# Performance work log

Measured on AMD Instinct MI355X. Metric: run time of the kernel, lower is better.

The kernel has to match this reference:

```python
import jax, jax.numpy as jnp
import numpy as np

DEPTH, DIM, HEADS, DH, MLP = 2, 512, 8, 64, 2048
INNER = HEADS * DH
B, L = 2, 2048
SCALE = DH ** -0.5
LN_EPS = 1e-5


def setup_inputs() -> dict:
    key = jax.random.key(0)
    ks = jax.random.split(key, 8)
    s = 0.02
    return {
        "x": jax.random.normal(ks[0], (B, L, DIM), dtype=jnp.float32),
        "mask": jax.random.randint(ks[1], (B, L, L), 0, 2, dtype=jnp.int32),
        "ln1_g": jnp.ones((DEPTH, DIM), jnp.float32),
        "ln1_b": jnp.zeros((DEPTH, DIM), jnp.float32),
        "w_qkv": jax.random.normal(ks[2], (DEPTH, DIM, 3 * INNER), jnp.float32) * s,
        "w_out": jax.random.normal(ks[3], (DEPTH, INNER, DIM), jnp.float32) * s,
        "b_out": jnp.zeros((DEPTH, DIM), jnp.float32),
        "ln2_g": jnp.ones((DEPTH, DIM), jnp.float32),
        "ln2_b": jnp.zeros((DEPTH, DIM), jnp.float32),
        "w1": jax.random.normal(ks[4], (DEPTH, DIM, MLP), jnp.float32) * s,
        "b1": jnp.zeros((DEPTH, MLP), jnp.float32),
        "w2": jax.random.normal(ks[5], (DEPTH, MLP, DIM), jnp.float32) * s,
        "b2": jnp.zeros((DEPTH, DIM), jnp.float32),
    }


def _layer_norm(x, g, b):
    m = jnp.mean(x, axis=-1, keepdims=True)
    v = jnp.mean(jnp.square(x - m), axis=-1, keepdims=True)
    return (x - m) * jax.lax.rsqrt(v + LN_EPS) * g + b


def _attention(h, mask_f, w_qkv, w_out, b_out):
    b, l, _ = h.shape
    qkv = h @ w_qkv  # [b,l,3*inner]
    qkv = qkv.reshape(b, l, 3, HEADS, DH)
    q = jnp.transpose(qkv[:, :, 0], (0, 2, 1, 3))  # [b,h,l,dh]
    k = jnp.transpose(qkv[:, :, 1], (0, 2, 1, 3))
    v = jnp.transpose(qkv[:, :, 2], (0, 2, 1, 3))
    scores = jnp.einsum('bhqd,bhkd->bhqk', q, k) * SCALE
    attn = jax.nn.softmax(scores, axis=-1)
    # multiplicative mask + renormalization (non-standard)
    attn = attn * mask_f
    attn = attn / (jnp.sum(attn, axis=-1, keepdims=True) + 1e-10)
    z = jnp.einsum('bhqk,bhkd->bhqd', attn, v)
    z = jnp.transpose(z, (0, 2, 1, 3)).reshape(b, l, INNER)
    return z @ w_out + b_out


def reference(x, mask, ln1_g, ln1_b, w_qkv, w_out, b_out, ln2_g, ln2_b, w1, b1, w2, b2):
    mask_f = mask[:, None, :, :].astype(x.dtype)  # [b,1,l,l]
    h = x
    for d in range(DEPTH):
        a = _attention(_layer_norm(h, ln1_g[d], ln1_b[d]), mask_f,
                       w_qkv[d], w_out[d], b_out[d])
        h = h + a
        f = _layer_norm(h, ln2_g[d], ln2_b[d])
        f = jax.nn.gelu(f @ w1[d] + b1[d], approximate=False) @ w2[d] + b2[d]
        h = h + f
    return h
```

## Files before the change

kernel.cpp:

```cpp
#include <hip/hip_runtime.h>
#include <math.h>

#define DEPTH 2
#define DIM   512
#define HEADS 8
#define DH    64
#define INNER 512
#define MLP_D 2048
#define BSZ   2
#define SEQ   2048
#define MROWS (BSZ*SEQ)
#define SCALE 0.125f
#define LN_EPS 1e-5f

typedef unsigned short u16;
typedef unsigned int   u32;
typedef __attribute__((ext_vector_type(8))) unsigned short u16x8;
typedef __attribute__((ext_vector_type(4))) unsigned short u16x4;
typedef __attribute__((ext_vector_type(8))) short          s16x8;
typedef __attribute__((ext_vector_type(4))) float          f32x4;

__device__ __forceinline__ u16 f2bf(float f) {
    u32 u = __float_as_uint(f);
    u += 0x7fffu + ((u >> 16) & 1u);
    return (u16)(u >> 16);
}

__device__ __forceinline__ float wred_sum(float v) {
    #pragma unroll
    for (int o = 32; o; o >>= 1) v += __shfl_xor(v, o);
    return v;
}

__global__ __launch_bounds__(256) void ln_kernel(
    const float* __restrict__ x,
    const float* __restrict__ g,
    const float* __restrict__ b,
    u16* __restrict__ y)
{
    const int wave = threadIdx.x >> 6;
    const int lane = threadIdx.x & 63;
    const int row  = blockIdx.x * 4 + wave;
    const float* xr = x + (size_t)row * DIM;

    float4 v0 = *reinterpret_cast<const float4*>(&xr[lane * 8]);
    float4 v1 = *reinterpret_cast<const float4*>(&xr[lane * 8 + 4]);

    float s = v0.x + v0.y + v0.z + v0.w + v1.x + v1.y + v1.z + v1.w;
    s = wred_sum(s);
    const float mean = s * (1.0f / DIM);

    float d[8] = {v0.x - mean, v0.y - mean, v0.z - mean, v0.w - mean,
                  v1.x - mean, v1.y - mean, v1.z - mean, v1.w - mean};
    float ss = 0.f;
    #pragma unroll
    for (int i = 0; i < 8; ++i) ss += d[i] * d[i];
    ss = wred_sum(ss);
    const float inv = rsqrtf(ss * (1.0f / DIM) + LN_EPS);

    float4 g0 = *reinterpret_cast<const float4*>(&g[lane * 8]);
    float4 g1 = *reinterpret_cast<const float4*>(&g[lane * 8 + 4]);
    float4 b0 = *reinterpret_cast<const float4*>(&b[lane * 8]);
    float4 b1 = *reinterpret_cast<const float4*>(&b[lane * 8 + 4]);
    const float gg[8] = {g0.x, g0.y, g0.z, g0.w, g1.x, g1.y, g1.z, g1.w};
    const float bb[8] = {b0.x, b0.y, b0.z, b0.w, b1.x, b1.y, b1.z, b1.w};

    u16x8 o;
    #pragma unroll
    for (int i = 0; i < 8; ++i) o[i] = f2bf(d[i] * inv * gg[i] + bb[i]);
    *reinterpret_cast<u16x8*>(&y[(size_t)row * DIM + lane * 8]) = o;
}

__global__ __launch_bounds__(256) void transpose_bf16_kernel(
    const float* __restrict__ in, u16* __restrict__ out, int K, int N)
{
    __shared__ u16 t[64][65];
    const int k0 = blockIdx.y * 64, n0 = blockIdx.x * 64;
    const int tid = threadIdx.x;
    #pragma unroll
    for (int i = 0; i < 4; ++i) {
        int idx = tid + i * 256;
        int r = idx >> 4, c4 = idx & 15;
        float4 v = *reinterpret_cast<const float4*>(&in[(size_t)(k0 + r) * N + n0 + c4 * 4]);
        t[c4 * 4 + 0][r] = f2bf(v.x);
        t[c4 * 4 + 1][r] = f2bf(v.y);
        t[c4 * 4 + 2][r] = f2bf(v.z);
        t[c4 * 4 + 3][r] = f2bf(v.w);
    }
    __syncthreads();
    #pragma unroll
    for (int i = 0; i < 2; ++i) {
        int idx = tid + i * 256;
        int r = idx >> 3, c8 = idx & 7;
        u16x8 w;
        #pragma unroll
        for (int j = 0; j < 8; ++j) w[j] = t[r][c8 * 8 + j];
        *reinterpret_cast<u16x8*>(&out[(size_t)(n0 + r) * K + k0 + c8 * 8]) = w;
    }
}

__global__ __launch_bounds__(256) void mask_pack_kernel(
    const int* __restrict__ mask, u32* __restrict__ mbT)
{
    const int wv = threadIdx.x >> 6, lane = threadIdx.x & 63;
    const int row = blockIdx.x * 4 + wv;
    const int b = row >> 11, l = row & (SEQ - 1);
    const int* mr = mask + (size_t)row * SEQ;
    u32* out = mbT + (size_t)b * 64 * SEQ;
    for (int it = 0; it < 32; ++it) {
        unsigned long long bal = __ballot(mr[it * 64 + lane] != 0);
        if (lane == 0) {
            out[(size_t)(2 * it) * SEQ + l]     = (u32)bal;
            out[(size_t)(2 * it + 1) * SEQ + l] = (u32)(bal >> 32);
        }
    }
}

template<int BM, int BN, int MT, int NT, int EPI>
__global__ __launch_bounds__(256) void gemm_bf16(
    const u16* __restrict__ A, const u16* __restrict__ BT,
    const float* __restrict__ bias, const float* __restrict__ Cin,
    void* __restrict__ CoutV, u16* __restrict__ qo, u16* __restrict__ ko,
    u16* __restrict__ vo, int M, int N, int K)
{
    constexpr int BK = 32;
    constexpr int LDW = 40;
    constexpr int WC = BN / (NT * 16);
    constexpr int AR = (BM * BK) / (256 * 8);
    constexpr int BR = (BN * BK) / (256 * 8);

    __shared__ __align__(16) u16 As[BM * LDW];
    __shared__ __align__(16) u16 Bs[BN * LDW];

    const int tid  = threadIdx.x;
    const int lane = tid & 63;
    const int wid  = tid >> 6;
    const int wr   = wid / WC, wc = wid % WC;
    const int lr   = lane & 15, lk = lane >> 4;
    const int bm   = blockIdx.y * BM, bn = blockIdx.x * BN;

    f32x4 acc[MT][NT];
    #pragma unroll
    for (int i = 0; i < MT; ++i)
        #pragma unroll
        for (int j = 0; j < NT; ++j) {
            acc[i][j][0] = 0.f; acc[i][j][1] = 0.f;
            acc[i][j][2] = 0.f; acc[i][j][3] = 0.f;
        }

    u16x8 ar[AR], br[BR];
    #pragma unroll
    for (int i = 0; i < AR; ++i) {
        int idx = tid + i * 256, row = idx >> 2, k16 = idx & 3;
        ar[i] = *reinterpret_cast<const u16x8*>(&A[(size_t)(bm + row) * K + k16 * 8]);
    }
    #pragma unroll
    for (int i = 0; i < BR; ++i) {
        int idx = tid + i * 256, row = idx >> 2, k16 = idx & 3;
        br[i] = *reinterpret_cast<const u16x8*>(&BT[(size_t)(bn + row) * K + k16 * 8]);
    }

    const int NTILES = K / BK;
    for (int t = 0; t < NTILES; ++t) {
        __syncthreads();
        #pragma unroll
        for (int i = 0; i < AR; ++i) {
            int idx = tid + i * 256, row = idx >> 2, k16 = idx & 3;
            *reinterpret_cast<u16x8*>(&As[row * LDW + k16 * 8]) = ar[i];
        }
        #pragma unroll
        for (int i = 0; i < BR; ++i) {
            int idx = tid + i * 256, row = idx >> 2, k16 = idx & 3;
            *reinterpret_cast<u16x8*>(&Bs[row * LDW + k16 * 8]) = br[i];
        }
        __syncthreads();

        if (t + 1 < NTILES) {
            const int k0 = (t + 1) * BK;
            #pragma unroll
            for (int i = 0; i < AR; ++i) {
                int idx = tid + i * 256, row = idx >> 2, k16 = idx & 3;
                ar[i] = *reinterpret_cast<const u16x8*>(&A[(size_t)(bm + row) * K + k0 + k16 * 8]);
            }
            #pragma unroll
            for (int i = 0; i < BR; ++i) {
                int idx = tid + i * 256, row = idx >> 2, k16 = idx & 3;
                br[i] = *reinterpret_cast<const u16x8*>(&BT[(size_t)(bn + row) * K + k0 + k16 * 8]);
            }
        }

        s16x8 af[MT], bf[NT];
        #pragma unroll
        for (int mt = 0; mt < MT; ++mt)
            af[mt] = *reinterpret_cast<const s16x8*>(&As[(wr * MT * 16 + mt * 16 + lr) * LDW + lk * 8]);
        #pragma unroll
        for (int nt = 0; nt < NT; ++nt)
            bf[nt] = *reinterpret_cast<const s16x8*>(&Bs[(wc * NT * 16 + nt * 16 + lr) * LDW + lk * 8]);
        #pragma unroll
        for (int mt = 0; mt < MT; ++mt)
            #pragma unroll
            for (int nt = 0; nt < NT; ++nt)
                acc[mt][nt] = __builtin_amdgcn_mfma_f32_16x16x32_bf16(
                    af[mt], bf[nt], acc[mt][nt], 0, 0, 0);
    }

    if (EPI == 3) {
        #pragma unroll
        for (int mt = 0; mt < MT; ++mt) {
            const int rbase = bm + wr * MT * 16 + mt * 16 + lk * 4;
            #pragma unroll
            for (int nt = 0; nt < NT; ++nt) {
                const int c = bn + wc * NT * 16 + nt * 16 + lr;
                const int sec = c >> 9, hh = (c >> 6) & 7, dd = c & 63;
                if (sec == 0) {
                    #pragma unroll
                    for (int i = 0; i < 4; ++i)
                        qo[((size_t)hh * MROWS + rbase + i) * 64 + dd] =
                            f2bf(acc[mt][nt][i] * SCALE);
                } else if (sec == 1) {
                    #pragma unroll
                    for (int i = 0; i < 4; ++i)
                        ko[((size_t)hh * MROWS + rbase + i) * 64 + dd] =
                            f2bf(acc[mt][nt][i]);
                } else {
                    u16x4 o;
                    #pragma unroll
                    for (int i = 0; i < 4; ++i) o[i] = f2bf(acc[mt][nt][i]);
                    *reinterpret_cast<u16x4*>(
                        &vo[((size_t)hh * 64 + dd) * MROWS + rbase]) = o;
                }
            }
        }
        return;
    }
    #pragma unroll
    for (int mt = 0; mt < MT; ++mt) {
        #pragma unroll
        for (int i = 0; i < 4; ++i) {
            const size_t r = bm + wr * MT * 16 + mt * 16 + lk * 4 + i;
            #pragma unroll
            for (int nt = 0; nt < NT; ++nt) {
                const size_t c = bn + wc * NT * 16 + nt * 16 + lr;
                float v = acc[mt][nt][i];
                if (EPI == 1) {
                    v += bias[c];
                    v = 0.5f * v * (1.0f + erff(v * 0.70710678118654752f));
                    ((u16*)CoutV)[r * N + c] = f2bf(v);
                } else {
                    v += bias[c] + Cin[r * N + c];
                    ((float*)CoutV)[r * N + c] = v;
                }
            }
        }
    }
}

__global__ __launch_bounds__(256) void attn_mfma_kernel(
    const u16* __restrict__ Qb,
    const u16* __restrict__ Kb,
    const u16* __restrict__ Vtb,
    const u32* __restrict__ mbT,
    u16* __restrict__ z)
{
    const int bh = blockIdx.y;
    const int b = bh >> 3, h = bh & 7;
    const int q0 = blockIdx.x * 64;
    const int tid = threadIdx.x;
    const int w = tid >> 6, lane = tid & 63;
    const int lr = lane & 15, lk = lane >> 4;

    __shared__ __align__(16) u16 Ks[128 * 72];
    __shared__ __align__(16) u16 Vts[64 * 136];

    const int qrow = q0 + w * 16 + lr;
    const size_t qg = (size_t)b * SEQ + qrow;

    s16x8 qf0, qf1;
    {
        const u16* Qrow = Qb + ((size_t)h * MROWS + qg) * 64;
        qf0 = *reinterpret_cast<const s16x8*>(Qrow + lk * 8);
        qf1 = *reinterpret_cast<const s16x8*>(Qrow + 32 + lk * 8);
    }

    float Mx = -1e30f, Sa = 0.f, Sm = 0.f;
    f32x4 zacc[4];
    #pragma unroll
    for (int dt = 0; dt < 4; ++dt) {
        zacc[dt][0] = 0.f; zacc[dt][1] = 0.f; zacc[dt][2] = 0.f; zacc[dt][3] = 0.f;
    }

    const u16* Kbase = Kb + ((size_t)h * MROWS + (size_t)b * SEQ) * 64;
    const u16* Vbase = Vtb + (size_t)h * 64 * MROWS + (size_t)b * SEQ;
    const u32* mbase = mbT + (size_t)b * 64 * SEQ;

    for (int kv0 = 0; kv0 < SEQ; kv0 += 128) {
        u16x8 kr[4], vr[4];
        #pragma unroll
        for (int i = 0; i < 4; ++i) {
            int idx = tid + i * 256;
            int row = idx >> 3, c8 = idx & 7;
            kr[i] = *reinterpret_cast<const u16x8*>(
                Kbase + (size_t)(kv0 + row) * 64 + c8 * 8);
        }
        #pragma unroll
        for (int i = 0; i < 4; ++i) {
            int idx = tid + i * 256;
            int row = idx >> 4, c = idx & 15;
            vr[i] = *reinterpret_cast<const u16x8*>(
                Vbase + (size_t)row * MROWS + kv0 + c * 8);
        }
        u32 mw[4];
        #pragma unroll
        for (int j = 0; j < 4; ++j)
            mw[j] = mbase[(size_t)(kv0 / 32 + j) * SEQ + qrow];

        __syncthreads();
        #pragma unroll
        for (int i = 0; i < 4; ++i) {
            int idx = tid + i * 256;
            int row = idx >> 3, c8 = idx & 7;
            *reinterpret_cast<u16x8*>(&Ks[row * 72 + c8 * 8]) = kr[i];
        }
        #pragma unroll
        for (int i = 0; i < 4; ++i) {
            int idx = tid + i * 256;
            int row = idx >> 4, c = idx & 15;
            *reinterpret_cast<u16x8*>(&Vts[row * 136 + c * 8]) = vr[i];
        }
        __syncthreads();

        f32x4 st[8];
        #pragma unroll
        for (int mt = 0; mt < 8; ++mt) {
            st[mt][0] = 0.f; st[mt][1] = 0.f; st[mt][2] = 0.f; st[mt][3] = 0.f;
        }
        #pragma unroll
        for (int mt = 0; mt < 8; ++mt) {
            const s16x8 a0 = *reinterpret_cast<const s16x8*>(
                &Ks[(mt * 16 + lr) * 72 + lk * 8]);
            const s16x8 a1 = *reinterpret_cast<const s16x8*>(
                &Ks[(mt * 16 + lr) * 72 + 32 + lk * 8]);
            st[mt] = __builtin_amdgcn_mfma_f32_16x16x32_bf16(a0, qf0, st[mt], 0, 0, 0);
            st[mt] = __builtin_amdgcn_mfma_f32_16x16x32_bf16(a1, qf1, st[mt], 0, 0, 0);
        }

        float ml = -1e30f;
        #pragma unroll
        for (int mt = 0; mt < 8; ++mt)
            #pragma unroll
            for (int i = 0; i < 4; ++i) ml = fmaxf(ml, st[mt][i]);
        ml = fmaxf(ml, __shfl_xor(ml, 16));
        ml = fmaxf(ml, __shfl_xor(ml, 32));
        const float Mn = fmaxf(Mx, ml);
        const float rsc = __expf(Mx - Mn);
        Mx = Mn;

        float ta = 0.f, tm = 0.f;
        #pragma unroll
        for (int mt = 0; mt < 8; ++mt) {
            const u32 wsh = mw[mt >> 1] >> ((mt & 1) * 16 + lk * 4);
            #pragma unroll
            for (int i = 0; i < 4; ++i) {
                float e = __expf(st[mt][i] - Mn);
                ta += e;
                float em = ((wsh >> i) & 1u) ? e : 0.f;
                tm += em;
                st[mt][i] = em;
            }
        }
        ta += __shfl_xor(ta, 16); ta += __shfl_xor(ta, 32);
        tm += __shfl_xor(tm, 16); tm += __shfl_xor(tm, 32);
        Sa = Sa * rsc + ta;
        Sm = Sm * rsc + tm;
        #pragma unroll
        for (int dt = 0; dt < 4; ++dt)
            #pragma unroll
            for (int i = 0; i < 4; ++i) zacc[dt][i] *= rsc;

        #pragma unroll
        for (int s = 0; s < 4; ++s) {
            s16x8 pf;
            #pragma unroll
            for (int i = 0; i < 4; ++i) {
                pf[i]     = (short)f2bf(st[2 * s][i]);
                pf[i + 4] = (short)f2bf(st[2 * s + 1][i]);
            }
            #pragma unroll
            for (int dt = 0; dt < 4; ++dt) {
                const u16* vrow = &Vts[(dt * 16 + lr) * 136 + s * 32 + lk * 4];
                u16x4 v0 = *reinterpret_cast<const u16x4*>(vrow);
                u16x4 v1 = *reinterpret_cast<const u16x4*>(vrow + 16);
                s16x8 av;
                #pragma unroll
                for (int i = 0; i < 4; ++i) {
                    av[i]     = (short)v0[i];
                    av[i + 4] = (short)v1[i];
                }
                zacc[dt] = __builtin_amdgcn_mfma_f32_16x16x32_bf16(av, pf, zacc[dt], 0, 0, 0);
            }
        }
    }

    const float inv = 1.0f / (Sm + 1e-10f * Sa);
    #pragma unroll
    for (int dt = 0; dt < 4; ++dt) {
        u16x4 o;
        #pragma unroll
        for (int i = 0; i < 4; ++i) o[i] = f2bf(zacc[dt][i] * inv);
        *reinterpret_cast<u16x4*>(
            &z[qg * INNER + h * 64 + dt * 16 + lk * 4]) = o;
    }
}

extern "C" void kernel_launch(void* const* d_in, const int* in_sizes, int n_in,
                              void* d_out, int out_size, void* d_ws, size_t ws_size,
                              hipStream_t stream) {
    const float* x      = (const float*)d_in[0];
    const int*   mask   = (const int*)  d_in[1];
    const float* ln1_g  = (const float*)d_in[2];
    const float* ln1_b  = (const float*)d_in[3];
    const float* w_qkv  = (const float*)d_in[4];
    const float* w_out  = (const float*)d_in[5];
    const float* b_out  = (const float*)d_in[6];
    const float* ln2_g  = (const float*)d_in[7];
    const float* ln2_b  = (const float*)d_in[8];
    const float* w1     = (const float*)d_in[9];
    const float* b1     = (const float*)d_in[10];
    const float* w2     = (const float*)d_in[11];
    const float* b2     = (const float*)d_in[12];

    float* h = (float*)d_out;

    u16* hn  = (u16*)d_ws;
    u16* zb  = hn + (size_t)MROWS * DIM;
    u32* mbT = (u32*)(zb + (size_t)MROWS * DIM);
    u16* wT  = (u16*)(mbT + (size_t)BSZ * 64 * SEQ);
    const size_t WT_LAYER = (size_t)DIM * 3 * INNER + (size_t)INNER * DIM
                          + (size_t)DIM * MLP_D + (size_t)MLP_D * DIM;
    u16* big = wT + DEPTH * WT_LAYER;
    u16* Qb  = big;
    u16* Kb  = Qb + (size_t)HEADS * MROWS * 64;
    u16* Vtb = Kb + (size_t)HEADS * MROWS * 64;
    u16* f1  = big;

    hipMemcpyAsync(h, x, (size_t)MROWS * DIM * sizeof(float),
                   hipMemcpyDeviceToDevice, stream);

    mask_pack_kernel<<<MROWS / 4, 256, 0, stream>>>(mask, mbT);
    for (int d = 0; d < DEPTH; ++d) {
        u16* wqkvT = wT + d * WT_LAYER;
        u16* woutT = wqkvT + (size_t)3 * INNER * DIM;
        u16* w1T   = woutT + (size_t)DIM * INNER;
        u16* w2T   = w1T   + (size_t)MLP_D * DIM;
        transpose_bf16_kernel<<<dim3(3 * INNER / 64, DIM / 64), 256, 0, stream>>>(
            w_qkv + (size_t)d * DIM * 3 * INNER, wqkvT, DIM, 3 * INNER);
        transpose_bf16_kernel<<<dim3(INNER / 64, DIM / 64), 256, 0, stream>>>(
            w_out + (size_t)d * INNER * DIM, woutT, INNER, DIM);
        transpose_bf16_kernel<<<dim3(MLP_D / 64, DIM / 64), 256, 0, stream>>>(
            w1 + (size_t)d * DIM * MLP_D, w1T, DIM, MLP_D);
        transpose_bf16_kernel<<<dim3(DIM / 64, MLP_D / 64), 256, 0, stream>>>(
            w2 + (size_t)d * MLP_D * DIM, w2T, MLP_D, DIM);
    }

    for (int d = 0; d < DEPTH; ++d) {
        u16* wqkvT = wT + d * WT_LAYER;
        u16* woutT = wqkvT + (size_t)3 * INNER * DIM;
        u16* w1T   = woutT + (size_t)DIM * INNER;
        u16* w2T   = w1T   + (size_t)MLP_D * DIM;

        ln_kernel<<<MROWS / 4, 256, 0, stream>>>(h, ln1_g + d * DIM, ln1_b + d * DIM, hn);

        gemm_bf16<128, 128, 4, 4, 3><<<dim3(3 * INNER / 128, MROWS / 128), 256, 0, stream>>>(
            hn, wqkvT, nullptr, nullptr, nullptr, Qb, Kb, Vtb, MROWS, 3 * INNER, DIM);

        attn_mfma_kernel<<<dim3(SEQ / 64, BSZ * HEADS), 256, 0, stream>>>(
            Qb, Kb, Vtb, mbT, zb);

        gemm_bf16<128, 64, 4, 2, 2><<<dim3(DIM / 64, MROWS / 128), 256, 0, stream>>>(
            zb, woutT, b_out + d * DIM, h, h, nullptr, nullptr, nullptr, MROWS, DIM, INNER);

        ln_kernel<<<MROWS / 4, 256, 0, stream>>>(h, ln2_g + d * DIM, ln2_b + d * DIM, hn);

        gemm_bf16<128, 128, 4, 4, 1><<<dim3(MLP_D / 128, MROWS / 128), 256, 0, stream>>>(
            hn, w1T, b1 + d * MLP_D, nullptr, f1, nullptr, nullptr, nullptr, MROWS, MLP_D, DIM);

        gemm_bf16<128, 64, 4, 2, 2><<<dim3(DIM / 64, MROWS / 128), 256, 0, stream>>>(
            f1, w2T, b2 + d * DIM, h, h, nullptr, nullptr, nullptr, MROWS, DIM, MLP_D);
    }
}
```

Baseline: 430.1 us.

## Double-buffer GEMM and attention tiles via direct global-to-LDS loads

GEMM and attention kernels now load tiles straight from global memory into LDS with global_load_lds into two buffers, so the next tile's loads overlap compute on the current one. K and V tiles use an XOR swizzle instead of padding, and V is stored in a permuted order so each MFMA operand comes from one 16-byte LDS read. Softmax moves to exp2 with log2e folded into the Q scale, rescales lazily only when the max grows by more than a threshold, uses packed bf16 conversion, and drops the unmasked sum from the denominator. That last change alters the epsilon term of the renormalisation, and the lazy rescale leaves exponentials unnormalised by up to 2^8.

```diff
diff --git a/kernel.cpp b/kernel.cpp
--- a/kernel.cpp
+++ b/kernel.cpp
@@ -11,6 +11,7 @@
 #define SEQ   2048
 #define MROWS (BSZ*SEQ)
 #define SCALE 0.125f
+#define QSC   0.18033688f
 #define LN_EPS 1e-5f
 
 typedef unsigned short u16;
@@ -25,6 +26,16 @@
     u += 0x7fffu + ((u >> 16) & 1u);
     return (u16)(u >> 16);
 }
+__device__ __forceinline__ u32 cvtpk(float lo, float hi) {
+    u32 r;
+    asm("v_cvt_pk_bf16_f32 %0, %1, %2" : "=v"(r) : "v"(lo), "v"(hi));
+    return r;
+}
+__device__ __forceinline__ void gld16(const void* g, void* l) {
+    __builtin_amdgcn_global_load_lds(
+        (const __attribute__((address_space(1))) void*)g,
+        (__attribute__((address_space(3))) void*)l, 16, 0, 0);
+}
 
 __device__ __forceinline__ float wred_sum(float v) {
     #pragma unroll
@@ -33,10 +44,8 @@
 }
 
 __global__ __launch_bounds__(256) void ln_kernel(
-    const float* __restrict__ x,
-    const float* __restrict__ g,
-    const float* __restrict__ b,
-    u16* __restrict__ y)
+    const float* __restrict__ x, const float* __restrict__ g,
+    const float* __restrict__ b, u16* __restrict__ y)
 {
     const int wave = threadIdx.x >> 6;
     const int lane = threadIdx.x & 63;
@@ -116,6 +125,22 @@
     }
 }
 
+#define GSTAGE(buf, kt) do {                                                   \
+    const int k0_ = (kt) * BK;                                                 \
+    _Pragma("unroll")                                                          \
+    for (int i_ = 0; i_ < ACH; ++i_) {                                         \
+        int idx_ = i_ * 256 + tid; int r_ = idx_ >> 2, kc_ = idx_ & 3;         \
+        gld16(&A[(size_t)(bm + r_) * K + k0_ + kc_ * 8],                       \
+              &As[buf][(size_t)(i_ * 256 + (wid << 6)) * 8]);                  \
+    }                                                                          \
+    _Pragma("unroll")                                                          \
+    for (int i_ = 0; i_ < BCH; ++i_) {                                         \
+        int idx_ = i_ * 256 + tid; int r_ = idx_ >> 2, kc_ = idx_ & 3;         \
+        gld16(&BT[(size_t)(bn + r_) * K + k0_ + kc_ * 8],                      \
+              &Bs[buf][(size_t)(i_ * 256 + (wid << 6)) * 8]);                  \
+    }                                                                          \
+} while (0)
+
 template<int BM, int BN, int MT, int NT, int EPI>
 __global__ __launch_bounds__(256) void gemm_bf16(
     const u16* __restrict__ A, const u16* __restrict__ BT,
@@ -124,20 +149,18 @@
     u16* __restrict__ vo, int M, int N, int K)
 {
     constexpr int BK = 32;
-    constexpr int LDW = 40;
     constexpr int WC = BN / (NT * 16);
-    constexpr int AR = (BM * BK) / (256 * 8);
-    constexpr int BR = (BN * BK) / (256 * 8);
-
-    __shared__ __align__(16) u16 As[BM * LDW];
-    __shared__ __align__(16) u16 Bs[BN * LDW];
+    constexpr int ACH = (BM * BK) / (256 * 8);
+    constexpr int BCH = (BN * BK) / (256 * 8);
+
+    __shared__ __align__(16) u16 As[2][BM * BK];
+    __shared__ __align__(16) u16 Bs[2][BN * BK];
 
     const int tid  = threadIdx.x;
-    const int lane = tid & 63;
-    const int wid  = tid >> 6;
-    const int wr   = wid / WC, wc = wid % WC;
-    const int lr   = lane & 15, lk = lane >> 4;
-    const int bm   = blockIdx.y * BM, bn = blockIdx.x * BN;
+    const int lane = tid & 63, wid = tid >> 6;
+    const int wr = wid / WC, wc = wid % WC;
+    const int lr = lane & 15, lk = lane >> 4;
+    const int bm = blockIdx.y * BM, bn = blockIdx.x * BN;
 
     f32x4 acc[MT][NT];
     #pragma unroll
@@ -148,60 +171,34 @@
             acc[i][j][2] = 0.f; acc[i][j][3] = 0.f;
         }
 
-    u16x8 ar[AR], br[BR];
-    #pragma unroll
-    for (int i = 0; i < AR; ++i) {
-        int idx = tid + i * 256, row = idx >> 2, k16 = idx & 3;
-        ar[i] = *reinterpret_cast<const u16x8*>(&A[(size_t)(bm + row) * K + k16 * 8]);
-    }
-    #pragma unroll
-    for (int i = 0; i < BR; ++i) {
-        int idx = tid + i * 256, row = idx >> 2, k16 = idx & 3;
-        br[i] = *reinterpret_cast<const u16x8*>(&BT[(size_t)(bn + row) * K + k16 * 8]);
-    }
+    GSTAGE(0, 0);
+    asm volatile("s_waitcnt vmcnt(0)" ::: "memory");
+    __syncthreads();
 
     const int NTILES = K / BK;
+    int cur = 0;
     for (int t = 0; t < NTILES; ++t) {
-        __syncthreads();
-        #pragma unroll
-        for (int i = 0; i < AR; ++i) {
-            int idx = tid + i * 256, row = idx >> 2, k16 = idx & 3;
-            *reinterpret_cast<u16x8*>(&As[row * LDW + k16 * 8]) = ar[i];
-        }
-        #pragma unroll
-        for (int i = 0; i < BR; ++i) {
-            int idx = tid + i * 256, row = idx >> 2, k16 = idx & 3;
-            *reinterpret_cast<u16x8*>(&Bs[row * LDW + k16 * 8]) = br[i];
-        }
-        __syncthreads();
-
-        if (t + 1 < NTILES) {
-            const int k0 = (t + 1) * BK;
-            #pragma unroll
-            for (int i = 0; i < AR; ++i) {
-                int idx = tid + i * 256, row = idx >> 2, k16 = idx & 3;
-                ar[i] = *reinterpret_cast<const u16x8*>(&A[(size_t)(bm + row) * K + k0 + k16 * 8]);
-            }
-            #pragma unroll
-            for (int i = 0; i < BR; ++i) {
-                int idx = tid + i * 256, row = idx >> 2, k16 = idx & 3;
-                br[i] = *reinterpret_cast<const u16x8*>(&BT[(size_t)(bn + row) * K + k0 + k16 * 8]);
-            }
-        }
+        if (t + 1 < NTILES) GSTAGE(cur ^ 1, t + 1);
 
         s16x8 af[MT], bf[NT];
         #pragma unroll
         for (int mt = 0; mt < MT; ++mt)
-            af[mt] = *reinterpret_cast<const s16x8*>(&As[(wr * MT * 16 + mt * 16 + lr) * LDW + lk * 8]);
+            af[mt] = *reinterpret_cast<const s16x8*>(
+                &As[cur][(wr * MT * 16 + mt * 16 + lr) * BK + lk * 8]);
         #pragma unroll
         for (int nt = 0; nt < NT; ++nt)
-            bf[nt] = *reinterpret_cast<const s16x8*>(&Bs[(wc * NT * 16 + nt * 16 + lr) * LDW + lk * 8]);
+            bf[nt] = *reinterpret_cast<const s16x8*>(
+                &Bs[cur][(wc * NT * 16 + nt * 16 + lr) * BK + lk * 8]);
         #pragma unroll
         for (int mt = 0; mt < MT; ++mt)
             #pragma unroll
             for (int nt = 0; nt < NT; ++nt)
                 acc[mt][nt] = __builtin_amdgcn_mfma_f32_16x16x32_bf16(
                     af[mt], bf[nt], acc[mt][nt], 0, 0, 0);
+
+        asm volatile("s_waitcnt vmcnt(0)" ::: "memory");
+        __syncthreads();
+        cur ^= 1;
     }
 
     if (EPI == 3) {
@@ -216,18 +213,19 @@
                     #pragma unroll
                     for (int i = 0; i < 4; ++i)
                         qo[((size_t)hh * MROWS + rbase + i) * 64 + dd] =
-                            f2bf(acc[mt][nt][i] * SCALE);
+                            f2bf(acc[mt][nt][i] * QSC);
                 } else if (sec == 1) {
                     #pragma unroll
                     for (int i = 0; i < 4; ++i)
                         ko[((size_t)hh * MROWS + rbase + i) * 64 + dd] =
                             f2bf(acc[mt][nt][i]);
                 } else {
+                    const int pos = (rbase & ~31) + lk * 8 + (mt & 1) * 4;
                     u16x4 o;
                     #pragma unroll
                     for (int i = 0; i < 4; ++i) o[i] = f2bf(acc[mt][nt][i]);
                     *reinterpret_cast<u16x4*>(
-                        &vo[((size_t)hh * 64 + dd) * MROWS + rbase]) = o;
+                        &vo[((size_t)hh * 64 + dd) * MROWS + pos]) = o;
                 }
             }
         }
@@ -254,6 +252,22 @@
         }
     }
 }
+#undef GSTAGE
+
+#define ASTAGE(buf, kv) do {                                                   \
+    _Pragma("unroll")                                                          \
+    for (int i_ = 0; i_ < 4; ++i_) {                                           \
+        int idx_ = i_ * 256 + tid; int r_ = idx_ >> 3, c_ = idx_ & 7;          \
+        gld16(Kbase + (size_t)((kv) + r_) * 64 + ((c_ ^ (r_ & 7)) * 8),        \
+              &Ks[buf][(size_t)(i_ * 256 + (wid << 6)) * 8]);                  \
+    }                                                                          \
+    _Pragma("unroll")                                                          \
+    for (int i_ = 0; i_ < 4; ++i_) {                                           \
+        int idx_ = i_ * 256 + tid; int r_ = idx_ >> 4, c_ = idx_ & 15;         \
+        gld16(Vbase + (size_t)r_ * MROWS + (kv) + ((c_ ^ (r_ & 7)) * 8),       \
+              &Vts[buf][(size_t)(i_ * 256 + (wid << 6)) * 8]);                 \
+    }                                                                          \
+} while (0)
 
 __global__ __launch_bounds__(256) void attn_mfma_kernel(
     const u16* __restrict__ Qb,
@@ -266,13 +280,14 @@
     const int b = bh >> 3, h = bh & 7;
     const int q0 = blockIdx.x * 64;
     const int tid = threadIdx.x;
-    const int w = tid >> 6, lane = tid & 63;
+    const int wid = tid >> 6, lane = tid & 63;
     const int lr = lane & 15, lk = lane >> 4;
-
-    __shared__ __align__(16) u16 Ks[128 * 72];
-    __shared__ __align__(16) u16 Vts[64 * 136];
-
-    const int qrow = q0 + w * 16 + lr;
+    const int lr7 = lr & 7;
+
+    __shared__ __align__(16) u16 Ks[2][128 * 64];
+    __shared__ __align__(16) u16 Vts[2][64 * 128];
+
+    const int qrow = q0 + wid * 16 + lr;
     const size_t qg = (size_t)b * SEQ + qrow;
 
     s16x8 qf0, qf1;
@@ -282,7 +297,7 @@
         qf1 = *reinterpret_cast<const s16x8*>(Qrow + 32 + lk * 8);
     }
 
-    float Mx = -1e30f, Sa = 0.f, Sm = 0.f;
+    float Mx = -1e30f, Sm = 0.f;
     f32x4 zacc[4];
     #pragma unroll
     for (int dt = 0; dt < 4; ++dt) {
@@ -293,42 +308,20 @@
     const u16* Vbase = Vtb + (size_t)h * 64 * MROWS + (size_t)b * SEQ;
     const u32* mbase = mbT + (size_t)b * 64 * SEQ;
 
-    for (int kv0 = 0; kv0 < SEQ; kv0 += 128) {
-        u16x8 kr[4], vr[4];
-        #pragma unroll
-        for (int i = 0; i < 4; ++i) {
-            int idx = tid + i * 256;
-            int row = idx >> 3, c8 = idx & 7;
-            kr[i] = *reinterpret_cast<const u16x8*>(
-                Kbase + (size_t)(kv0 + row) * 64 + c8 * 8);
-        }
-        #pragma unroll
-        for (int i = 0; i < 4; ++i) {
-            int idx = tid + i * 256;
-            int row = idx >> 4, c = idx & 15;
-            vr[i] = *reinterpret_cast<const u16x8*>(
-                Vbase + (size_t)row * MROWS + kv0 + c * 8);
-        }
+    ASTAGE(0, 0);
+    asm volatile("s_waitcnt vmcnt(0)" ::: "memory");
+    __syncthreads();
+
+    int cur = 0;
+    for (int t = 0; t < SEQ / 128; ++t) {
+        if (t + 1 < SEQ / 128) ASTAGE(cur ^ 1, (t + 1) * 128);
+
         u32 mw[4];
         #pragma unroll
         for (int j = 0; j < 4; ++j)
-            mw[j] = mbase[(size_t)(kv0 / 32 + j) * SEQ + qrow];
-
-        __syncthreads();
-        #pragma unroll
-        for (int i = 0; i < 4; ++i) {
-            int idx = tid + i * 256;
-            int row = idx >> 3, c8 = idx & 7;
-            *reinterpret_cast<u16x8*>(&Ks[row * 72 + c8 * 8]) = kr[i];
-        }
-        #pragma unroll
-        for (int i = 0; i < 4; ++i) {
-            int idx = tid + i * 256;
-            int row = idx >> 4, c = idx & 15;
-            *reinterpret_cast<u16x8*>(&Vts[row * 136 + c * 8]) = vr[i];
-        }
-        __syncthreads();
-
+            mw[j] = mbase[(size_t)(t * 4 + j) * SEQ + qrow];
+
+        const u16* Kc = Ks[cur];
         f32x4 st[8];
         #pragma unroll
         for (int mt = 0; mt < 8; ++mt) {
@@ -337,71 +330,68 @@
         #pragma unroll
         for (int mt = 0; mt < 8; ++mt) {
             const s16x8 a0 = *reinterpret_cast<const s16x8*>(
-                &Ks[(mt * 16 + lr) * 72 + lk * 8]);
+                &Kc[(mt * 16 + lr) * 64 + ((lk ^ lr7) * 8)]);
             const s16x8 a1 = *reinterpret_cast<const s16x8*>(
-                &Ks[(mt * 16 + lr) * 72 + 32 + lk * 8]);
+                &Kc[(mt * 16 + lr) * 64 + (((lk + 4) ^ lr7) * 8)]);
             st[mt] = __builtin_amdgcn_mfma_f32_16x16x32_bf16(a0, qf0, st[mt], 0, 0, 0);
             st[mt] = __builtin_amdgcn_mfma_f32_16x16x32_bf16(a1, qf1, st[mt], 0, 0, 0);
         }
 
-        float ml = -1e30f;
+        float ml = st[0][0];
         #pragma unroll
         for (int mt = 0; mt < 8; ++mt)
             #pragma unroll
             for (int i = 0; i < 4; ++i) ml = fmaxf(ml, st[mt][i]);
         ml = fmaxf(ml, __shfl_xor(ml, 16));
         ml = fmaxf(ml, __shfl_xor(ml, 32));
-        const float Mn = fmaxf(Mx, ml);
-        const float rsc = __expf(Mx - Mn);
-        Mx = Mn;
-
-        float ta = 0.f, tm = 0.f;
+        if (__any(ml > Mx + 8.f)) {
+            const float Mn = fmaxf(Mx, ml);
+            const float r  = exp2f(Mx - Mn);
+            Sm *= r;
+            #pragma unroll
+            for (int dt = 0; dt < 4; ++dt)
+                #pragma unroll
+                for (int i = 0; i < 4; ++i) zacc[dt][i] *= r;
+            Mx = Mn;
+        }
+        float tm = 0.f;
         #pragma unroll
         for (int mt = 0; mt < 8; ++mt) {
-            const u32 wsh = mw[mt >> 1] >> ((mt & 1) * 16 + lk * 4);
+            const u32 wsh = mw[mt >> 1] >> (((mt & 1) << 4) | (lk << 2));
             #pragma unroll
             for (int i = 0; i < 4; ++i) {
-                float e = __expf(st[mt][i] - Mn);
-                ta += e;
-                float em = ((wsh >> i) & 1u) ? e : 0.f;
-                tm += em;
-                st[mt][i] = em;
+                float e = exp2f(st[mt][i] - Mx);
+                e = ((wsh >> i) & 1u) ? e : 0.f;
+                st[mt][i] = e;
+                tm += e;
             }
         }
-        ta += __shfl_xor(ta, 16); ta += __shfl_xor(ta, 32);
-        tm += __shfl_xor(tm, 16); tm += __shfl_xor(tm, 32);
-        Sa = Sa * rsc + ta;
-        Sm = Sm * rsc + tm;
-        #pragma unroll
-        for (int dt = 0; dt < 4; ++dt)
-            #pragma unroll
-            for (int i = 0; i < 4; ++i) zacc[dt][i] *= rsc;
-
+        tm += __shfl_xor(tm, 16);
+        tm += __shfl_xor(tm, 32);
+        Sm += tm;
+
+        const u16* Vc = Vts[cur];
         #pragma unroll
         for (int s = 0; s < 4; ++s) {
-            s16x8 pf;
-            #pragma unroll
-            for (int i = 0; i < 4; ++i) {
-                pf[i]     = (short)f2bf(st[2 * s][i]);
-                pf[i + 4] = (short)f2bf(st[2 * s + 1][i]);
+            union { u32 w[4]; s16x8 v; } pu;
+            pu.w[0] = cvtpk(st[2 * s][0], st[2 * s][1]);
+            pu.w[1] = cvtpk(st[2 * s][2], st[2 * s][3]);
+            pu.w[2] = cvtpk(st[2 * s + 1][0], st[2 * s + 1][1]);
+            pu.w[3] = cvtpk(st[2 * s + 1][2], st[2 * s + 1][3]);
+            #pragma unroll
+            for (int dt = 0; dt < 4; ++dt) {
+                const s16x8 av = *reinterpret_cast<const s16x8*>(
+                    &Vc[(dt * 16 + lr) * 128 + (((s * 4 + lk) ^ lr7) * 8)]);
+                zacc[dt] = __builtin_amdgcn_mfma_f32_16x16x32_bf16(av, pu.v, zacc[dt], 0, 0, 0);
             }
-            #pragma unroll
-            for (int dt = 0; dt < 4; ++dt) {
-                const u16* vrow = &Vts[(dt * 16 + lr) * 136 + s * 32 + lk * 4];
-                u16x4 v0 = *reinterpret_cast<const u16x4*>(vrow);
-                u16x4 v1 = *reinterpret_cast<const u16x4*>(vrow + 16);
-                s16x8 av;
-                #pragma unroll
-                for (int i = 0; i < 4; ++i) {
-                    av[i]     = (short)v0[i];
-                    av[i + 4] = (short)v1[i];
-                }
-                zacc[dt] = __builtin_amdgcn_mfma_f32_16x16x32_bf16(av, pf, zacc[dt], 0, 0, 0);
-            }
-        }
-    }
-
-    const float inv = 1.0f / (Sm + 1e-10f * Sa);
+        }
+
+        asm volatile("s_waitcnt vmcnt(0)" ::: "memory");
+        __syncthreads();
+        cur ^= 1;
+    }
+
+    const float inv = 1.0f / (Sm + 1e-10f);
     #pragma unroll
     for (int dt = 0; dt < 4; ++dt) {
         u16x4 o;
@@ -411,6 +401,7 @@
             &z[qg * INNER + h * 64 + dt * 16 + lk * 4]) = o;
     }
 }
+#undef ASTAGE
 
 extern "C" void kernel_launch(void* const* d_in, const int* in_sizes, int n_in,
                               void* d_out, int out_size, void* d_ws, size_t ws_size,
```

After: 439.6 us. 2.2% more time.
